# Kernel optimization log

Hardware: AMD Instinct MI355X
Metric: run time of the kernel (lower is better)

## Reference

```python
import jax, jax.numpy as jnp
import numpy as np

B, NF, NU = 8, 64, 1024
DF, DU, DH, H = 64, 32, 128, 8


def setup_inputs() -> dict:
    key = jax.random.key(0)
    ks = jax.random.split(key, 10)
    s = 0.05  # keep logits in a stable range
    return {
        "f0": jax.random.normal(ks[0], (B, NF, DF), jnp.float32),
        "u0": jax.random.normal(ks[1], (B, NU, DU), jnp.float32),
        "f1": jax.random.normal(ks[2], (B, NF, DF), jnp.float32),
        "u1": jax.random.normal(ks[3], (B, NU, DU), jnp.float32),
        "Wf": jax.random.normal(ks[4], (H, 2, 3, DF, DH), jnp.float32) * s,
        "bf": jax.random.normal(ks[5], (H, 2, 3, DH), jnp.float32) * s,
        "Wu": jax.random.normal(ks[6], (H, 2, 3, DU, DH), jnp.float32) * s,
        "bu": jax.random.normal(ks[7], (H, 2, 3, DH), jnp.float32) * s,
        "Wout": jax.random.normal(ks[8], (H * DH, DH), jnp.float32) * s,
        "bout": jax.random.normal(ks[9], (DH,), jnp.float32) * s,
    }


def _proj(x, W, b):
    # x: [B,N,Din], W: [H,3,Din,DH], b: [H,3,DH] -> [3,B,H,N,DH] (qkv-major)
    y = jnp.einsum('bnf,hkfd->kbhnd', x, W)
    return y + b.transpose(1, 0, 2)[:, None, :, None, :]


def reference(f0, u0, f1, u1, Wf, bf, Wu, bu, Wout, bout):
    # per-head per-player Q/K/V projections; concat order: [f0, u0, f1, u1]
    parts = [
        _proj(f0, Wf[:, 0], bf[:, 0]),
        _proj(u0, Wu[:, 0], bu[:, 0]),
        _proj(f1, Wf[:, 1], bf[:, 1]),
        _proj(u1, Wu[:, 1], bu[:, 1]),
    ]
    qkv = jnp.concatenate(parts, axis=3)  # [3,B,H,S,DH]
    Q, K, V = qkv[0], qkv[1], qkv[2]
    scale = jnp.asarray(DH ** 0.5, Q.dtype)
    scores = jnp.einsum('bhqd,bhkd->bhqk', Q, K) / scale  # [B,H,S,S]
    attn = jax.nn.softmax(scores, axis=-1)
    out = jnp.einsum('bhqk,bhkd->bhqd', attn, V)  # [B,H,S,DH]
    # concat heads along feature dim (head order preserved), then final linear
    S = out.shape[2]
    out = out.transpose(0, 2, 1, 3).reshape(out.shape[0], S, H * DH)
    return out @ Wout + bout  # [B,S,DH]
```

## Files before the change

### kernel.cpp

```cpp
#include <hip/hip_runtime.h>
#include <hip/hip_bf16.h>

#define BB 8
#define NFQ 64
#define NUQ 1024
#define HH 8
#define SS 2176

typedef __attribute__((ext_vector_type(8))) short short8;
typedef __attribute__((ext_vector_type(4))) float f32x4;
typedef __attribute__((ext_vector_type(2))) unsigned int uint2_t;
typedef unsigned short ubf;

__device__ __forceinline__ ubf f2bf(float x) {
    unsigned u = __float_as_uint(x);
    u = u + 0x7fffu + ((u >> 16) & 1u);
    return (ubf)(u >> 16);
}
__device__ __forceinline__ unsigned pkbf(float a, float b) {
    __hip_bfloat162 h = __float22bfloat162_rn(make_float2(a, b));
    union { __hip_bfloat162 hh; unsigned u; } c; c.hh = h;
    return c.u;
}
__device__ __forceinline__ float bf2f(short v) {
    return __uint_as_float(((unsigned)(ubf)v) << 16);
}

__global__ __launch_bounds__(256) void prep_kernel(
    const float* __restrict__ Wf, const float* __restrict__ Wu, const float* __restrict__ Wout,
    ubf* __restrict__ WfT, ubf* __restrict__ WuT, ubf* __restrict__ WoutT)
{
    __shared__ ubf tl[128 * 72];
    const int idx = blockIdx.x, tid = threadIdx.x;
    const float* src; ubf* dst; int F, dstride;
    if (idx < 48)       { F = 64; src = Wf + (size_t)idx * 64 * 128;        dst = WfT + (size_t)idx * 128 * 64;        dstride = 64; }
    else if (idx < 96)  { F = 32; src = Wu + (size_t)(idx - 48) * 32 * 128; dst = WuT + (size_t)(idx - 48) * 128 * 32; dstride = 32; }
    else                { F = 64; int s = idx - 96; src = Wout + (size_t)s * 64 * 128; dst = WoutT + s * 64; dstride = 1024; }
    const int pitch = F + 8;
    for (int i = tid; i < F * 32; i += 256) {
        int f = i >> 5, d0 = (i & 31) * 4;
        f32x4 v = *(const f32x4*)&src[f * 128 + d0];
        tl[(d0 + 0) * pitch + f] = f2bf(v[0]);
        tl[(d0 + 1) * pitch + f] = f2bf(v[1]);
        tl[(d0 + 2) * pitch + f] = f2bf(v[2]);
        tl[(d0 + 3) * pitch + f] = f2bf(v[3]);
    }
    __syncthreads();
    if (F == 64) {
        int d = tid >> 1, half = tid & 1;
#pragma unroll
        for (int jj = 0; jj < 4; ++jj)
            *(short8*)&dst[(size_t)d * dstride + half * 32 + jj * 8] =
                *(const short8*)&tl[d * pitch + half * 32 + jj * 8];
    } else {
        int d = tid & 127, fh = tid >> 7;
#pragma unroll
        for (int jj = 0; jj < 2; ++jj)
            *(short8*)&dst[(size_t)d * dstride + fh * 16 + jj * 8] =
                *(const short8*)&tl[d * pitch + fh * 16 + jj * 8];
    }
}

__global__ __launch_bounds__(256) void proj_kernel(
    const float* __restrict__ f0, const float* __restrict__ u0,
    const float* __restrict__ f1, const float* __restrict__ u1,
    const ubf* __restrict__ WfT, const ubf* __restrict__ WuT,
    const float* __restrict__ bfv, const float* __restrict__ buv,
    ubf* __restrict__ Qg, ubf* __restrict__ Kg, ubf* __restrict__ Vtg)
{
    __shared__ ubf xlds[32 * 64];
    __shared__ ubf outq[32 * 136];
    __shared__ ubf outk[32 * 136];
    __shared__ ubf outv[128 * 40];

    const int tid = threadIdx.x;
    const int bh = blockIdx.x / 17, j = blockIdx.x % 17;
    const int b = bh >> 3, h = bh & 7;
    const int w = tid >> 6, l = tid & 63, lg = l >> 4, dl = l & 15;
    const int dg0 = w * 2;

    const bool isF = (j == 0);
    const f32x4 zf = {0.f, 0.f, 0.f, 0.f};

    short8 af[3][2][2];
    f32x4 bv[3][2];

    const int up = isF ? 0 : ((j - 1) >> 3);
    const int ugrp = isF ? 0 : ((j - 1) & 7);
    const float* xpb = 0;
    if (!isF) xpb = (up ? u1 : u0) + (size_t)b * NUQ * 32;

    for (int c4 = 0; c4 < 4; ++c4) {
        int p, n0, s0;
        const float* xp;
        if (isF) {
            p = c4 >> 1; n0 = (c4 & 1) * 32;
            s0 = p ? 1088 + (c4 & 1) * 32 : (c4 & 1) * 32;
            xp = (p ? f1 : f0) + (size_t)b * NFQ * 64;
        } else {
            p = up; int c = ugrp * 4 + c4; n0 = 32 * c;
            s0 = (p ? 1152 : 64) + 32 * c;
            xp = xpb;
        }

        if (c4 == 0 || (isF && c4 == 2)) {
            if (isF) {
                const ubf* wt = WfT + (size_t)((h * 2 + p) * 3) * 8192;
#pragma unroll
                for (int k = 0; k < 3; ++k)
#pragma unroll
                    for (int g = 0; g < 2; ++g) {
                        af[k][g][0] = *(const short8*)&wt[(size_t)k * 8192 + ((dg0 + g) * 16 + dl) * 64 + lg * 8];
                        af[k][g][1] = *(const short8*)&wt[(size_t)k * 8192 + ((dg0 + g) * 16 + dl) * 64 + 32 + lg * 8];
                        bv[k][g] = *(const f32x4*)&bfv[((h * 2 + p) * 3 + k) * 128 + (dg0 + g) * 16 + 4 * lg];
                    }
            } else {
                const ubf* wt = WuT + (size_t)((h * 2 + p) * 3) * 4096;
#pragma unroll
                for (int k = 0; k < 3; ++k)
#pragma unroll
                    for (int g = 0; g < 2; ++g) {
                        af[k][g][0] = *(const short8*)&wt[(size_t)k * 4096 + ((dg0 + g) * 16 + dl) * 32 + lg * 8];
                        bv[k][g] = *(const f32x4*)&buv[((h * 2 + p) * 3 + k) * 128 + (dg0 + g) * 16 + 4 * lg];
                    }
            }
        }

        if (isF) {
            int row = tid >> 3, g = tid & 7;
            const float* s = &xp[(size_t)(n0 + row) * 64 + g * 8];
            f32x4 v0 = *(const f32x4*)&s[0];
            f32x4 v1 = *(const f32x4*)&s[4];
            union { unsigned u[4]; short8 s8; } pk;
            pk.u[0] = pkbf(v0[0], v0[1]); pk.u[1] = pkbf(v0[2], v0[3]);
            pk.u[2] = pkbf(v1[0], v1[1]); pk.u[3] = pkbf(v1[2], v1[3]);
            *(short8*)&xlds[row * 64 + ((g ^ (row & 7)) * 8)] = pk.s8;
        } else if (tid < 128) {
            int row = tid >> 2, g = tid & 3;
            const float* s = &xp[(size_t)(n0 + row) * 32 + g * 8];
            f32x4 v0 = *(const f32x4*)&s[0];
            f32x4 v1 = *(const f32x4*)&s[4];
            union { unsigned u[4]; short8 s8; } pk;
            pk.u[0] = pkbf(v0[0], v0[1]); pk.u[1] = pkbf(v0[2], v0[3]);
            pk.u[2] = pkbf(v1[0], v1[1]); pk.u[3] = pkbf(v1[2], v1[3]);
            *(short8*)&xlds[row * 64 + ((g ^ (row & 7)) * 8)] = pk.s8;
        }
        __syncthreads();

        short8 bx0[2], bx1[2];
#pragma unroll
        for (int tile = 0; tile < 2; ++tile) {
            const int row = tile * 16 + dl;
            bx0[tile] = *(const short8*)&xlds[row * 64 + ((lg ^ (row & 7)) * 8)];
            if (isF)
                bx1[tile] = *(const short8*)&xlds[row * 64 + (((4 + lg) ^ (row & 7)) * 8)];
        }

#pragma unroll
        for (int k = 0; k < 3; ++k)
#pragma unroll
            for (int g = 0; g < 2; ++g)
#pragma unroll
                for (int tile = 0; tile < 2; ++tile) {
                    f32x4 acc = __builtin_amdgcn_mfma_f32_16x16x32_bf16(af[k][g][0], bx0[tile], zf, 0, 0, 0);
                    if (isF)
                        acc = __builtin_amdgcn_mfma_f32_16x16x32_bf16(af[k][g][1], bx1[tile], acc, 0, 0, 0);
                    if (k < 2) {
                        ubf* o = k ? outk : outq;
                        uint2_t wv;
                        wv.x = pkbf(acc[0] + bv[k][g][0], acc[1] + bv[k][g][1]);
                        wv.y = pkbf(acc[2] + bv[k][g][2], acc[3] + bv[k][g][3]);
                        *(uint2_t*)&o[(tile * 16 + dl) * 136 + (dg0 + g) * 16 + 4 * lg] = wv;
                    } else {
                        int pos = (dl & 3) + 8 * ((dl >> 2) & 3) + 4 * tile;
#pragma unroll
                        for (int r = 0; r < 4; ++r)
                            outv[((dg0 + g) * 16 + 4 * lg + r) * 40 + pos] = f2bf(acc[r] + bv[2][g][r]);
                    }
                }
        __syncthreads();

        {
            int row = tid >> 3, c16 = (tid & 7) * 16;
            size_t qbase = ((size_t)bh * SS + s0 + row) * 128 + c16;
            *(short8*)&Qg[qbase]     = *(const short8*)&outq[row * 136 + c16];
            *(short8*)&Qg[qbase + 8] = *(const short8*)&outq[row * 136 + c16 + 8];
            *(short8*)&Kg[qbase]     = *(const short8*)&outk[row * 136 + c16];
            *(short8*)&Kg[qbase + 8] = *(const short8*)&outk[row * 136 + c16 + 8];
            int dd = tid >> 1, half = tid & 1;
            size_t vbase = ((size_t)bh * 128 + dd) * SS + s0 + half * 16;
            *(short8*)&Vtg[vbase]     = *(const short8*)&outv[dd * 40 + half * 16];
            *(short8*)&Vtg[vbase + 8] = *(const short8*)&outv[dd * 40 + half * 16 + 8];
        }
    }
}

__global__ __launch_bounds__(512) void attn_kernel(
    const ubf* __restrict__ Qg, const ubf* __restrict__ Kg, const ubf* __restrict__ Vtg,
    ubf* __restrict__ attnout)
{
    __shared__ ubf Klds[2][64 * 128];
    __shared__ ubf Vlds[2][128 * 64];

    const int tid = threadIdx.x;
    const int swz = (blockIdx.x & 7) * 72 + (blockIdx.x >> 3);
    const int bh = swz / 9;
    const int qc = swz % 9;
    const int b = bh >> 3, h = bh & 7;
    const int w = tid >> 6, l = tid & 63, lg = l >> 4, dl = l & 15;
    int qbase = qc * 256 + w * 32;
    const bool qvalid = qbase < SS;
    if (!qvalid) qbase = SS - 32;
    const int qr0 = qbase + dl;

    const ubf* Qbh = Qg + (size_t)bh * SS * 128;
    const ubf* Kbh = Kg + (size_t)bh * SS * 128;
    const ubf* Vbh = Vtg + (size_t)bh * 128 * SS;

    short8 qfa[4], qfb[4];
#pragma unroll
    for (int dc = 0; dc < 4; ++dc) {
        qfa[dc] = *(const short8*)&Qbh[(size_t)qr0 * 128 + dc * 32 + lg * 8];
        qfb[dc] = *(const short8*)&Qbh[(size_t)(qr0 + 16) * 128 + dc * 32 + lg * 8];
    }

    f32x4 otA[8], otB[8];
    const f32x4 zf = {0.f, 0.f, 0.f, 0.f};
#pragma unroll
    for (int i = 0; i < 8; ++i) { otA[i] = zf; otB[i] = zf; }
    float lsA = 0.f, lsB = 0.f;

    const int skrow = tid >> 3, skc = tid & 7;
    const int svrow = tid >> 2, svc = tid & 3;
    const float sc = 0.08838834764831845f * 1.44269504088896340736f;

    const int ksw = (skrow & 7) << 3;
    const int ko0 = skrow * 128 + ((skc * 16) ^ ksw);
    const int ko1 = skrow * 128 + ((skc * 16 + 8) ^ ksw);
    const int vr7 = svrow & 7;
    const int vo0 = svrow * 64 + (((2 * svc)     ^ vr7) * 8);
    const int vo1 = svrow * 64 + (((2 * svc + 1) ^ vr7) * 8);
    const ubf* kp = &Kbh[(size_t)skrow * 128 + skc * 16];
    const ubf* vp = &Vbh[(size_t)svrow * SS + svc * 16];
    const int pvs = (dl & 7) << 3;

    short8 k0s, k1s, v0s, v1s;
    k0s = *(const short8*)&kp[0];
    k1s = *(const short8*)&kp[8];
    v0s = *(const short8*)&vp[0];
    v1s = *(const short8*)&vp[8];
    *(short8*)&Klds[0][ko0] = k0s;
    *(short8*)&Klds[0][ko1] = k1s;
    *(short8*)&Vlds[0][vo0] = v0s;
    *(short8*)&Vlds[0][vo1] = v1s;
    __syncthreads();

    int cur = 0;
    for (int it = 0; it < 34; ++it) {
        if (it < 33) {
            const size_t nb = (size_t)(it + 1) * 64;
            k0s = *(const short8*)&kp[nb * 128];
            k1s = *(const short8*)&kp[nb * 128 + 8];
            v0s = *(const short8*)&vp[nb];
            v1s = *(const short8*)&vp[nb + 8];
        }
        const ubf* Kc = Klds[cur];
        const ubf* Vc = Vlds[cur];

        f32x4 s0a = zf, s1a = zf, s0b = zf, s1b = zf;
        f32x4 t0a = zf, t1a = zf, t0b = zf, t1b = zf;
        __builtin_amdgcn_s_setprio(1);
#pragma unroll
        for (int dc = 0; dc < 4; ++dc) {
            const int col = (dc * 32 + lg * 8) ^ pvs;
            short8 k0 = *(const short8*)&Kc[dl * 128 + col];
            short8 k1 = *(const short8*)&Kc[(16 + dl) * 128 + col];
            short8 k2 = *(const short8*)&Kc[(32 + dl) * 128 + col];
            short8 k3 = *(const short8*)&Kc[(48 + dl) * 128 + col];
            s0a = __builtin_amdgcn_mfma_f32_16x16x32_bf16(k0, qfa[dc], s0a, 0, 0, 0);
            s1a = __builtin_amdgcn_mfma_f32_16x16x32_bf16(k1, qfa[dc], s1a, 0, 0, 0);
            t0a = __builtin_amdgcn_mfma_f32_16x16x32_bf16(k2, qfa[dc], t0a, 0, 0, 0);
            t1a = __builtin_amdgcn_mfma_f32_16x16x32_bf16(k3, qfa[dc], t1a, 0, 0, 0);
            s0b = __builtin_amdgcn_mfma_f32_16x16x32_bf16(k0, qfb[dc], s0b, 0, 0, 0);
            s1b = __builtin_amdgcn_mfma_f32_16x16x32_bf16(k1, qfb[dc], s1b, 0, 0, 0);
            t0b = __builtin_amdgcn_mfma_f32_16x16x32_bf16(k2, qfb[dc], t0b, 0, 0, 0);
            t1b = __builtin_amdgcn_mfma_f32_16x16x32_bf16(k3, qfb[dc], t1b, 0, 0, 0);
        }
        __builtin_amdgcn_s_setprio(0);

        union { unsigned u[4]; short8 s; } Pa0, Pa1, Pb0, Pb1;
#define EXPPACK(lo, hi, P, lsum) { \
            float e0 = __builtin_amdgcn_exp2f(lo[0] * sc); \
            float e1 = __builtin_amdgcn_exp2f(lo[1] * sc); \
            float e2 = __builtin_amdgcn_exp2f(lo[2] * sc); \
            float e3 = __builtin_amdgcn_exp2f(lo[3] * sc); \
            float e4 = __builtin_amdgcn_exp2f(hi[0] * sc); \
            float e5 = __builtin_amdgcn_exp2f(hi[1] * sc); \
            float e6 = __builtin_amdgcn_exp2f(hi[2] * sc); \
            float e7 = __builtin_amdgcn_exp2f(hi[3] * sc); \
            lsum += ((e0 + e1) + (e2 + e3)) + ((e4 + e5) + (e6 + e7)); \
            P.u[0] = pkbf(e0, e1); P.u[1] = pkbf(e2, e3); \
            P.u[2] = pkbf(e4, e5); P.u[3] = pkbf(e6, e7); }
        EXPPACK(s0a, s1a, Pa0, lsA);
        EXPPACK(t0a, t1a, Pa1, lsA);
        EXPPACK(s0b, s1b, Pb0, lsB);
        EXPPACK(t0b, t1b, Pb1, lsB);
#undef EXPPACK

        __builtin_amdgcn_s_setprio(1);
#pragma unroll
        for (int dt = 0; dt < 8; ++dt) {
            const int vrow = (dt * 16 + dl) * 64;
            short8 vf0 = *(const short8*)&Vc[vrow + ((lg * 8) ^ pvs)];
            short8 vf1 = *(const short8*)&Vc[vrow + (((4 + lg) * 8) ^ pvs)];
            otA[dt] = __builtin_amdgcn_mfma_f32_16x16x32_bf16(vf0, Pa0.s, otA[dt], 0, 0, 0);
            otA[dt] = __builtin_amdgcn_mfma_f32_16x16x32_bf16(vf1, Pa1.s, otA[dt], 0, 0, 0);
            otB[dt] = __builtin_amdgcn_mfma_f32_16x16x32_bf16(vf0, Pb0.s, otB[dt], 0, 0, 0);
            otB[dt] = __builtin_amdgcn_mfma_f32_16x16x32_bf16(vf1, Pb1.s, otB[dt], 0, 0, 0);
        }
        __builtin_amdgcn_s_setprio(0);

        if (it < 33) {
            ubf* Kn = Klds[cur ^ 1];
            ubf* Vn = Vlds[cur ^ 1];
            *(short8*)&Kn[ko0] = k0s;
            *(short8*)&Kn[ko1] = k1s;
            *(short8*)&Vn[vo0] = v0s;
            *(short8*)&Vn[vo1] = v1s;
            cur ^= 1;
            __syncthreads();
        }
    }

    if (qvalid) {
        lsA += __shfl_xor(lsA, 16); lsA += __shfl_xor(lsA, 32);
        lsB += __shfl_xor(lsB, 16); lsB += __shfl_xor(lsB, 32);
        const float invA = 1.f / lsA, invB = 1.f / lsB;

        ubf* dstA = attnout + ((size_t)b * SS + qr0) * 1024 + h * 128;
        ubf* dstB = attnout + ((size_t)b * SS + qr0 + 16) * 1024 + h * 128;
#pragma unroll
        for (int dt = 0; dt < 8; ++dt) {
            f32x4 oA = otA[dt] * invA;
            f32x4 oB = otB[dt] * invB;
            uint2_t wA, wB;
            wA.x = pkbf(oA[0], oA[1]); wA.y = pkbf(oA[2], oA[3]);
            wB.x = pkbf(oB[0], oB[1]); wB.y = pkbf(oB[2], oB[3]);
            *(uint2_t*)&dstA[dt * 16 + 4 * lg] = wA;
            *(uint2_t*)&dstB[dt * 16 + 4 * lg] = wB;
        }
    }
}

__global__ __launch_bounds__(256) void outproj_kernel(
    const ubf* __restrict__ attnout, const ubf* __restrict__ WoutT,
    const float* __restrict__ bout, float* __restrict__ out)
{
    __shared__ ubf alds[32 * 1024];
    const int tid = threadIdx.x;
    const int row0 = blockIdx.x * 32;
    const int w = tid >> 6, l = tid & 63, lg = l >> 4, dl = l & 15;
    const int dg0 = w * 2;
    const f32x4 zf = {0.f, 0.f, 0.f, 0.f};

#pragma unroll
    for (int pz = 0; pz < 2; ++pz) {
        int row = pz * 16 + (tid >> 4);
        int cl = tid & 15;
#pragma unroll
        for (int jj = 0; jj < 8; ++jj) {
            int g = cl + 16 * jj;
            short8 v = *(const short8*)&attnout[(size_t)(row0 + row) * 1024 + g * 8];
            *(short8*)&alds[row * 1024 + ((g ^ (row & 7)) * 8)] = v;
        }
    }
    __syncthreads();

    f32x4 acc[2][2];
    acc[0][0] = zf; acc[0][1] = zf; acc[1][0] = zf; acc[1][1] = zf;

    for (int dc = 0; dc < 32; ++dc) {
        short8 a0 = *(const short8*)&WoutT[(size_t)((dg0 + 0) * 16 + dl) * 1024 + dc * 32 + lg * 8];
        short8 a1 = *(const short8*)&WoutT[(size_t)((dg0 + 1) * 16 + dl) * 1024 + dc * 32 + lg * 8];
        short8 b0 = *(const short8*)&alds[dl * 1024 + (((dc * 4 + lg) ^ (dl & 7)) * 8)];
        short8 b1 = *(const short8*)&alds[(16 + dl) * 1024 + (((dc * 4 + lg) ^ (dl & 7)) * 8)];
        acc[0][0] = __builtin_amdgcn_mfma_f32_16x16x32_bf16(a0, b0, acc[0][0], 0, 0, 0);
        acc[0][1] = __builtin_amdgcn_mfma_f32_16x16x32_bf16(a0, b1, acc[0][1], 0, 0, 0);
        acc[1][0] = __builtin_amdgcn_mfma_f32_16x16x32_bf16(a1, b0, acc[1][0], 0, 0, 0);
        acc[1][1] = __builtin_amdgcn_mfma_f32_16x16x32_bf16(a1, b1, acc[1][1], 0, 0, 0);
    }

#pragma unroll
    for (int g = 0; g < 2; ++g) {
        f32x4 bb = *(const f32x4*)&bout[(dg0 + g) * 16 + 4 * lg];
#pragma unroll
        for (int tile = 0; tile < 2; ++tile) {
            f32x4 o = acc[g][tile] + bb;
            *(f32x4*)&out[((size_t)row0 + tile * 16 + dl) * 128 + (dg0 + g) * 16 + 4 * lg] = o;
        }
    }
}

extern "C" void kernel_launch(void* const* d_in, const int* in_sizes, int n_in,
                              void* d_out, int out_size, void* d_ws, size_t ws_size,
                              hipStream_t stream) {
    const float* f0  = (const float*)d_in[0];
    const float* u0  = (const float*)d_in[1];
    const float* f1  = (const float*)d_in[2];
    const float* u1  = (const float*)d_in[3];
    const float* Wf  = (const float*)d_in[4];
    const float* bfv = (const float*)d_in[5];
    const float* Wu  = (const float*)d_in[6];
    const float* buv = (const float*)d_in[7];
    const float* Wout = (const float*)d_in[8];
    const float* bout = (const float*)d_in[9];
    float* out = (float*)d_out;

    char* ws = (char*)d_ws;
    const size_t qkv_bytes = (size_t)BB * HH * SS * 128 * sizeof(ubf);
    ubf* Qg  = (ubf*)ws;
    ubf* Kg  = (ubf*)(ws + qkv_bytes);
    ubf* Vtg = (ubf*)(ws + 2 * qkv_bytes);
    ubf* attnout = (ubf*)(ws + 3 * qkv_bytes);
    ubf* WfT   = (ubf*)(ws + 4 * qkv_bytes);
    ubf* WuT   = (ubf*)(ws + 4 * qkv_bytes + 786432);
    ubf* WoutT = (ubf*)(ws + 4 * qkv_bytes + 786432 + 393216);

    prep_kernel<<<dim3(112), dim3(256), 0, stream>>>(Wf, Wu, Wout, WfT, WuT, WoutT);
    proj_kernel<<<dim3(64 * 17), dim3(256), 0, stream>>>(f0, u0, f1, u1, WfT, WuT, bfv, buv, Qg, Kg, Vtg);
    attn_kernel<<<dim3(576), dim3(512), 0, stream>>>(Qg, Kg, Vtg, attnout);
    outproj_kernel<<<dim3(544), dim3(256), 0, stream>>>(attnout, WoutT, bout, out);
}
```

Baseline: 275.4 us.

## Read K and V tiles directly from global memory instead of LDS double-buffering

Removes the shared-memory double-buffered staging of K and V tiles in the attention kernel. Each wave now loads its MFMA operands straight from global memory (relying on L1/L2 to serve the reuse across the 8 waves), which eliminates the LDS stores, swizzle arithmetic and per-iteration block barriers. The trade-off is much more global/cache traffic per block, since all 8 waves re-read the same K/V data, and there is no explicit prefetch to hide load latency.

```diff
diff --git a/kernel.cpp b/kernel.cpp
--- a/kernel.cpp
+++ b/kernel.cpp
@@ -199,9 +199,6 @@
     const ubf* __restrict__ Qg, const ubf* __restrict__ Kg, const ubf* __restrict__ Vtg,
     ubf* __restrict__ attnout)
 {
-    __shared__ ubf Klds[2][64 * 128];
-    __shared__ ubf Vlds[2][128 * 64];
-
     const int tid = threadIdx.x;
     const int swz = (blockIdx.x & 7) * 72 + (blockIdx.x >> 3);
     const int bh = swz / 9;
@@ -230,53 +227,21 @@
     for (int i = 0; i < 8; ++i) { otA[i] = zf; otB[i] = zf; }
     float lsA = 0.f, lsB = 0.f;
 
-    const int skrow = tid >> 3, skc = tid & 7;
-    const int svrow = tid >> 2, svc = tid & 3;
     const float sc = 0.08838834764831845f * 1.44269504088896340736f;
 
-    const int ksw = (skrow & 7) << 3;
-    const int ko0 = skrow * 128 + ((skc * 16) ^ ksw);
-    const int ko1 = skrow * 128 + ((skc * 16 + 8) ^ ksw);
-    const int vr7 = svrow & 7;
-    const int vo0 = svrow * 64 + (((2 * svc)     ^ vr7) * 8);
-    const int vo1 = svrow * 64 + (((2 * svc + 1) ^ vr7) * 8);
-    const ubf* kp = &Kbh[(size_t)skrow * 128 + skc * 16];
-    const ubf* vp = &Vbh[(size_t)svrow * SS + svc * 16];
-    const int pvs = (dl & 7) << 3;
-
-    short8 k0s, k1s, v0s, v1s;
-    k0s = *(const short8*)&kp[0];
-    k1s = *(const short8*)&kp[8];
-    v0s = *(const short8*)&vp[0];
-    v1s = *(const short8*)&vp[8];
-    *(short8*)&Klds[0][ko0] = k0s;
-    *(short8*)&Klds[0][ko1] = k1s;
-    *(short8*)&Vlds[0][vo0] = v0s;
-    *(short8*)&Vlds[0][vo1] = v1s;
-    __syncthreads();
-
-    int cur = 0;
     for (int it = 0; it < 34; ++it) {
-        if (it < 33) {
-            const size_t nb = (size_t)(it + 1) * 64;
-            k0s = *(const short8*)&kp[nb * 128];
-            k1s = *(const short8*)&kp[nb * 128 + 8];
-            v0s = *(const short8*)&vp[nb];
-            v1s = *(const short8*)&vp[nb + 8];
-        }
-        const ubf* Kc = Klds[cur];
-        const ubf* Vc = Vlds[cur];
+        const size_t kb = (size_t)it * 64;
 
         f32x4 s0a = zf, s1a = zf, s0b = zf, s1b = zf;
         f32x4 t0a = zf, t1a = zf, t0b = zf, t1b = zf;
         __builtin_amdgcn_s_setprio(1);
 #pragma unroll
         for (int dc = 0; dc < 4; ++dc) {
-            const int col = (dc * 32 + lg * 8) ^ pvs;
-            short8 k0 = *(const short8*)&Kc[dl * 128 + col];
-            short8 k1 = *(const short8*)&Kc[(16 + dl) * 128 + col];
-            short8 k2 = *(const short8*)&Kc[(32 + dl) * 128 + col];
-            short8 k3 = *(const short8*)&Kc[(48 + dl) * 128 + col];
+            const ubf* kcol = &Kbh[(kb + dl) * 128 + dc * 32 + lg * 8];
+            short8 k0 = *(const short8*)&kcol[0];
+            short8 k1 = *(const short8*)&kcol[16 * 128];
+            short8 k2 = *(const short8*)&kcol[32 * 128];
+            short8 k3 = *(const short8*)&kcol[48 * 128];
             s0a = __builtin_amdgcn_mfma_f32_16x16x32_bf16(k0, qfa[dc], s0a, 0, 0, 0);
             s1a = __builtin_amdgcn_mfma_f32_16x16x32_bf16(k1, qfa[dc], s1a, 0, 0, 0);
             t0a = __builtin_amdgcn_mfma_f32_16x16x32_bf16(k2, qfa[dc], t0a, 0, 0, 0);
@@ -310,26 +275,15 @@
         __builtin_amdgcn_s_setprio(1);
 #pragma unroll
         for (int dt = 0; dt < 8; ++dt) {
-            const int vrow = (dt * 16 + dl) * 64;
-            short8 vf0 = *(const short8*)&Vc[vrow + ((lg * 8) ^ pvs)];
-            short8 vf1 = *(const short8*)&Vc[vrow + (((4 + lg) * 8) ^ pvs)];
+            const ubf* vrow = &Vbh[(size_t)(dt * 16 + dl) * SS + kb];
+            short8 vf0 = *(const short8*)&vrow[lg * 8];
+            short8 vf1 = *(const short8*)&vrow[32 + lg * 8];
             otA[dt] = __builtin_amdgcn_mfma_f32_16x16x32_bf16(vf0, Pa0.s, otA[dt], 0, 0, 0);
             otA[dt] = __builtin_amdgcn_mfma_f32_16x16x32_bf16(vf1, Pa1.s, otA[dt], 0, 0, 0);
             otB[dt] = __builtin_amdgcn_mfma_f32_16x16x32_bf16(vf0, Pb0.s, otB[dt], 0, 0, 0);
             otB[dt] = __builtin_amdgcn_mfma_f32_16x16x32_bf16(vf1, Pb1.s, otB[dt], 0, 0, 0);
         }
         __builtin_amdgcn_s_setprio(0);
-
-        if (it < 33) {
-            ubf* Kn = Klds[cur ^ 1];
-            ubf* Vn = Vlds[cur ^ 1];
-            *(short8*)&Kn[ko0] = k0s;
-            *(short8*)&Kn[ko1] = k1s;
-            *(short8*)&Vn[vo0] = v0s;
-            *(short8*)&Vn[vo1] = v1s;
-            cur ^= 1;
-            __syncthreads();
-        }
     }
 
     if (qvalid) {
```

After: 793.3 us. 2.88x slower.
